# Optimization experiments

Hardware: AMD Instinct MI355X
Metric: run time of the kernel (lower is better)

## Reference

```python
import jax, jax.numpy as jnp
import numpy as np

M, K, N = 4096, 4096, 4096          # tokens, in_features, out_features
ROW_BLOCK, COL_BLOCK = 1, 4          # sparse block shape (rows x cols of W)
BLOCK_DENSITY = 0.2                  # fraction of nonzero blocks


def setup_inputs() -> dict:
    key = jax.random.key(0)
    k1, k2, k3, k4 = jax.random.split(key, 4)
    # quint8 activations stored as int32 in [0, 255]
    x_q = jax.random.randint(k1, (M, K), 0, 256, dtype=jnp.int32)
    # qint8 weights stored as int32 in [-127, 127], zero_point == 0
    w_dense = jax.random.randint(k2, (N, K), -127, 128, dtype=jnp.int32)
    # block-sparse structure: zero out whole ROW_BLOCK x COL_BLOCK blocks
    blk_mask = jax.random.bernoulli(k3, BLOCK_DENSITY, (N // ROW_BLOCK, K // COL_BLOCK))
    mask = jnp.repeat(jnp.repeat(blk_mask, ROW_BLOCK, axis=0), COL_BLOCK, axis=1)
    w_q = jnp.where(mask, w_dense, 0)
    bias = jax.random.normal(k4, (N,), dtype=jnp.float32) * 0.1
    return dict(
        x_q=x_q,
        w_q=w_q,
        bias=bias,
        x_scale=jnp.float32(0.05),
        x_zp=jnp.int32(128),
        w_scale=jnp.float32(0.01),
        out_scale=jnp.float32(0.1),
        out_zp=jnp.int32(128),
    )


def reference(x_q, w_q, bias, x_scale, x_zp, w_scale, out_scale, out_zp):
    # int32 accumulate of (x - x_zp) @ W^T over the (block-)sparse weight
    acc = jnp.einsum('mk,nk->mn', x_q - x_zp, w_q)  # [M, N] int32
    # dequantize + bias
    y = acc.astype(jnp.float32) * (x_scale * w_scale) + bias[None, :]
    # requantize to quint8 (stored as int32)
    q = jnp.round(y / out_scale).astype(jnp.int32) + out_zp
    return jnp.clip(q, 0, 255)
```

## Files before the change

### kernel.cpp

```cpp
#include <hip/hip_runtime.h>
#include <stdint.h>

#define MDIM 4096
#define NDIM 4096
#define KDIM 4096
#define BM 256
#define BN 256
#define BKB 128
#define NT (KDIM / BKB)

typedef int i32x4 __attribute__((ext_vector_type(4)));

typedef __attribute__((address_space(1))) const void gv_t;
typedef __attribute__((address_space(3))) void lv_t;

#define BAR() do { asm volatile("" ::: "memory"); __builtin_amdgcn_s_barrier(); asm volatile("" ::: "memory"); } while (0)

__device__ __forceinline__ int pack4(int a, int b, int c, int d) {
    return (a & 0xFF) | ((b & 0xFF) << 8) | ((c & 0xFF) << 16) | ((d & 0xFF) << 24);
}

__global__ void pack_x_kernel(const int* __restrict__ x, const int* __restrict__ zp_p,
                              int* __restrict__ out, int total4) {
    const int zp = zp_p[0];
    int i = blockIdx.x * blockDim.x + threadIdx.x;
    if (i < total4) {
        int4 a = ((const int4*)x)[i];
        out[i] = pack4(a.x - zp, a.y - zp, a.z - zp, a.w - zp);
    }
}

__global__ void pack_w_kernel(const int* __restrict__ w, int* __restrict__ out, int total4) {
    int i = blockIdx.x * blockDim.x + threadIdx.x;
    if (i < total4) {
        int4 a = ((const int4*)w)[i];
        out[i] = pack4(a.x, a.y, a.z, a.w);
    }
}

__global__ __launch_bounds__(512, 2)
void gemm_i8_8ph(const char* __restrict__ A8, const char* __restrict__ B8,
                 const float* __restrict__ bias,
                 const float* __restrict__ xs_p, const float* __restrict__ ws_p,
                 const float* __restrict__ os_p, const int* __restrict__ ozp_p,
                 int* __restrict__ out) {
    __shared__ char lds[131072];

    const int t = threadIdx.x;
    const int lane = t & 63;
    const int wave = t >> 6;
    const int wr = wave >> 2;
    const int wc = wave & 3;

    int wg = blockIdx.x;
    int swz = (wg & 7) * (256 / 8) + (wg >> 3);
    const long brow = (long)(swz >> 4) * BM;
    const long bcol = (long)(swz & 15) * BN;

    i32x4 acc[8][4] = {};

    auto STAGE_HALF = [&](int tt, int h) {
        if (tt >= NT) return;
        const int d = tt & 1;
        const char* src = (h < 2) ? A8 : B8;
        const long base_rc = (h < 2) ? brow : bcol;
        const int rh = h & 1;
        const int kt = tt * BKB;
        char* ldsbase = lds + ((h < 2) ? 0 : 65536) + d * 32768;
        #pragma unroll
        for (int j = 0; j < 2; ++j) {
            int chunk = rh * 1024 + t + j * 512;
            int row = chunk >> 3, slot = chunk & 7;
            __builtin_amdgcn_global_load_lds(
                (gv_t*)(src + (base_rc + row) * KDIM + kt + ((slot ^ (row & 7)) * 16)),
                (lv_t*)(ldsbase + chunk * 16), 16, 0, 0);
        }
    };

    STAGE_HALF(0, 0); STAGE_HALF(0, 1); STAGE_HALF(0, 2); STAGE_HALF(0, 3);
    STAGE_HALF(1, 0); STAGE_HALF(1, 1); STAGE_HALF(1, 2);

    for (int tt = 0; tt < NT; ++tt) {
        const int d = tt & 1;
        const char* Ac = lds + d * 32768;
        const char* Bc = lds + 65536 + d * 32768;

        STAGE_HALF(tt + 1, 3);
        if (tt == NT - 1) asm volatile("s_waitcnt vmcnt(0)" ::: "memory");
        else              asm volatile("s_waitcnt vmcnt(8)" ::: "memory");
        BAR();

        i32x4 af[8][2], bf[4][2];
        #pragma unroll
        for (int mi = 0; mi < 8; ++mi) {
            int row = wr * 128 + mi * 16 + (lane & 15);
            #pragma unroll
            for (int kk = 0; kk < 2; ++kk) {
                int ls = kk * 4 + (lane >> 4);
                af[mi][kk] = *(const i32x4*)(Ac + row * BKB + ((ls ^ (row & 7)) * 16));
            }
        }
        #pragma unroll
        for (int ni = 0; ni < 4; ++ni) {
            int row = wc * 64 + ni * 16 + (lane & 15);
            #pragma unroll
            for (int kk = 0; kk < 2; ++kk) {
                int ls = kk * 4 + (lane >> 4);
                bf[ni][kk] = *(const i32x4*)(Bc + row * BKB + ((ls ^ (row & 7)) * 16));
            }
        }

        __builtin_amdgcn_s_setprio(1);
        #pragma unroll
        for (int mi = 0; mi < 4; ++mi)
            #pragma unroll
            for (int ni = 0; ni < 2; ++ni)
                #pragma unroll
                for (int kk = 0; kk < 2; ++kk)
                    acc[mi][ni] = __builtin_amdgcn_mfma_i32_16x16x64_i8(af[mi][kk], bf[ni][kk], acc[mi][ni], 0, 0, 0);
        __builtin_amdgcn_s_setprio(0);
        asm volatile("s_waitcnt lgkmcnt(0)" ::: "memory");
        BAR();

        STAGE_HALF(tt + 2, 0);
        BAR();
        __builtin_amdgcn_s_setprio(1);
        #pragma unroll
        for (int mi = 0; mi < 4; ++mi)
            #pragma unroll
            for (int ni = 2; ni < 4; ++ni)
                #pragma unroll
                for (int kk = 0; kk < 2; ++kk)
                    acc[mi][ni] = __builtin_amdgcn_mfma_i32_16x16x64_i8(af[mi][kk], bf[ni][kk], acc[mi][ni], 0, 0, 0);
        __builtin_amdgcn_s_setprio(0);
        BAR();

        STAGE_HALF(tt + 2, 1);
        BAR();
        __builtin_amdgcn_s_setprio(1);
        #pragma unroll
        for (int mi = 4; mi < 8; ++mi)
            #pragma unroll
            for (int ni = 0; ni < 2; ++ni)
                #pragma unroll
                for (int kk = 0; kk < 2; ++kk)
                    acc[mi][ni] = __builtin_amdgcn_mfma_i32_16x16x64_i8(af[mi][kk], bf[ni][kk], acc[mi][ni], 0, 0, 0);
        __builtin_amdgcn_s_setprio(0);
        BAR();

        STAGE_HALF(tt + 2, 2);
        BAR();
        __builtin_amdgcn_s_setprio(1);
        #pragma unroll
        for (int mi = 4; mi < 8; ++mi)
            #pragma unroll
            for (int ni = 2; ni < 4; ++ni)
                #pragma unroll
                for (int kk = 0; kk < 2; ++kk)
                    acc[mi][ni] = __builtin_amdgcn_mfma_i32_16x16x64_i8(af[mi][kk], bf[ni][kk], acc[mi][ni], 0, 0, 0);
        __builtin_amdgcn_s_setprio(0);
        BAR();
    }

    const float scale = xs_p[0] * ws_p[0];
    const float os = os_p[0];
    const int ozp = ozp_p[0];
    #pragma unroll
    for (int mi = 0; mi < 8; ++mi) {
        long row0 = brow + wr * 128 + mi * 16 + (lane >> 4) * 4;
        #pragma unroll
        for (int ni = 0; ni < 4; ++ni) {
            long col = bcol + wc * 64 + ni * 16 + (lane & 15);
            float bv = bias[col];
            #pragma unroll
            for (int r = 0; r < 4; ++r) {
                float y = (float)acc[mi][ni][r] * scale + bv;
                int q = (int)rintf(y / os) + ozp;
                q = q < 0 ? 0 : (q > 255 ? 255 : q);
                out[(row0 + r) * NDIM + col] = q;
            }
        }
    }
}

__global__ void naive_gemm_kernel(const int* __restrict__ x, const int* __restrict__ w,
                                  const float* __restrict__ bias,
                                  const float* __restrict__ xs_p, const int* __restrict__ xzp_p,
                                  const float* __restrict__ ws_p, const float* __restrict__ os_p,
                                  const int* __restrict__ ozp_p, int* __restrict__ out) {
    long idx = (long)blockIdx.x * blockDim.x + threadIdx.x;
    if (idx >= (long)MDIM * NDIM) return;
    int m = idx >> 12, n = idx & (NDIM - 1);
    const int4* xr = (const int4*)(x + (long)m * KDIM);
    const int4* wv = (const int4*)(w + (long)n * KDIM);
    const int zp = xzp_p[0];
    int acc = 0;
    for (int k = 0; k < KDIM / 4; ++k) {
        int4 a = xr[k], b = wv[k];
        acc += (a.x - zp) * b.x + (a.y - zp) * b.y + (a.z - zp) * b.z + (a.w - zp) * b.w;
    }
    float y = (float)acc * (xs_p[0] * ws_p[0]) + bias[n];
    int q = (int)rintf(y / os_p[0]) + ozp_p[0];
    out[idx] = q < 0 ? 0 : (q > 255 ? 255 : q);
}

extern "C" void kernel_launch(void* const* d_in, const int* in_sizes, int n_in,
                              void* d_out, int out_size, void* d_ws, size_t ws_size,
                              hipStream_t stream) {
    const int*   x_q  = (const int*)d_in[0];
    const int*   w_q  = (const int*)d_in[1];
    const float* bias = (const float*)d_in[2];
    const float* xs   = (const float*)d_in[3];
    const int*   xzp  = (const int*)d_in[4];
    const float* wsc  = (const float*)d_in[5];
    const float* osc  = (const float*)d_in[6];
    const int*   ozp  = (const int*)d_in[7];
    int* out = (int*)d_out;

    const size_t need = 2UL * MDIM * KDIM;
    if (ws_size >= need) {
        char* A8 = (char*)d_ws;
        char* B8 = A8 + (size_t)MDIM * KDIM;
        const int total4 = MDIM * KDIM / 4;
        pack_x_kernel<<<total4 / 256, 256, 0, stream>>>(x_q, xzp, (int*)A8, total4);
        pack_w_kernel<<<total4 / 256, 256, 0, stream>>>(w_q, (int*)B8, total4);
        gemm_i8_8ph<<<(MDIM / BM) * (NDIM / BN), 512, 0, stream>>>(
            A8, B8, bias, xs, wsc, osc, ozp, out);
    } else {
        long total = (long)MDIM * NDIM;
        naive_gemm_kernel<<<(total + 255) / 256, 256, 0, stream>>>(
            x_q, w_q, bias, xs, xzp, wsc, osc, ozp, out);
    }
}
```

Baseline: 236.4 us.

## Interleave LDS fragment loads with MFMA quarters and reorder tile staging

Restructures the main loop so A and B fragments are read from LDS in pieces just before the MFMA quarter that uses them, instead of all at once at the top of each iteration. The global-to-LDS staging order also changes: B halves for the next tile and A halves for the tile after next are issued between quarters, with adjusted vmcnt waits. Swizzled LDS and global addresses are precomputed outside the loop, and the loop is unrolled by two. The aim is to overlap LDS reads with MFMA work, lower peak register use and cut per-iteration address arithmetic. The cost is more barriers and lgkmcnt waits per iteration, and more complex correctness reasoning about buffer reuse.

```diff
diff --git a/kernel.cpp b/kernel.cpp
--- a/kernel.cpp
+++ b/kernel.cpp
@@ -15,6 +15,7 @@
 typedef __attribute__((address_space(3))) void lv_t;
 
 #define BAR() do { asm volatile("" ::: "memory"); __builtin_amdgcn_s_barrier(); asm volatile("" ::: "memory"); } while (0)
+#define LGKM0_BAR() do { asm volatile("s_waitcnt lgkmcnt(0)" ::: "memory"); BAR(); } while (0)
 
 __device__ __forceinline__ int pack4(int a, int b, int c, int d) {
     return (a & 0xFF) | ((b & 0xFF) << 8) | ((c & 0xFF) << 16) | ((d & 0xFF) << 24);
@@ -59,108 +60,116 @@
 
     i32x4 acc[8][4] = {};
 
-    auto STAGE_HALF = [&](int tt, int h) {
-        if (tt >= NT) return;
-        const int d = tt & 1;
+    int aoff[8][2], boff[4][2];
+    #pragma unroll
+    for (int mi = 0; mi < 8; ++mi) {
+        int row = wr * 128 + mi * 16 + (lane & 15);
+        #pragma unroll
+        for (int kk = 0; kk < 2; ++kk) {
+            int ls = kk * 4 + (lane >> 4);
+            aoff[mi][kk] = row * BKB + ((ls ^ (row & 7)) * 16);
+        }
+    }
+    #pragma unroll
+    for (int ni = 0; ni < 4; ++ni) {
+        int row = wc * 64 + ni * 16 + (lane & 15);
+        #pragma unroll
+        for (int kk = 0; kk < 2; ++kk) {
+            int ls = kk * 4 + (lane >> 4);
+            boff[ni][kk] = 65536 + row * BKB + ((ls ^ (row & 7)) * 16);
+        }
+    }
+    const char* sbase[4][2];
+    int ldsoff[4][2];
+    #pragma unroll
+    for (int h = 0; h < 4; ++h) {
         const char* src = (h < 2) ? A8 : B8;
-        const long base_rc = (h < 2) ? brow : bcol;
-        const int rh = h & 1;
-        const int kt = tt * BKB;
-        char* ldsbase = lds + ((h < 2) ? 0 : 65536) + d * 32768;
+        long rc = (h < 2) ? brow : bcol;
         #pragma unroll
         for (int j = 0; j < 2; ++j) {
-            int chunk = rh * 1024 + t + j * 512;
+            int chunk = (h & 1) * 1024 + t + j * 512;
             int row = chunk >> 3, slot = chunk & 7;
-            __builtin_amdgcn_global_load_lds(
-                (gv_t*)(src + (base_rc + row) * KDIM + kt + ((slot ^ (row & 7)) * 16)),
-                (lv_t*)(ldsbase + chunk * 16), 16, 0, 0);
-        }
-    };
-
-    STAGE_HALF(0, 0); STAGE_HALF(0, 1); STAGE_HALF(0, 2); STAGE_HALF(0, 3);
-    STAGE_HALF(1, 0); STAGE_HALF(1, 1); STAGE_HALF(1, 2);
-
+            sbase[h][j] = src + (rc + row) * KDIM + ((slot ^ (row & 7)) * 16);
+            ldsoff[h][j] = ((h < 2) ? 0 : 65536) + chunk * 16;
+        }
+    }
+
+#define STAGE(tt_, h_) do { \
+    if ((tt_) < NT) { \
+        int dd_ = ((tt_) & 1) * 32768; \
+        __builtin_amdgcn_global_load_lds((gv_t*)(sbase[h_][0] + (long)(tt_) * BKB), \
+                                         (lv_t*)(lds + dd_ + ldsoff[h_][0]), 16, 0, 0); \
+        __builtin_amdgcn_global_load_lds((gv_t*)(sbase[h_][1] + (long)(tt_) * BKB), \
+                                         (lv_t*)(lds + dd_ + ldsoff[h_][1]), 16, 0, 0); \
+    } } while (0)
+
+#define MFMA_Q(MLO, NLO) do { \
+    __builtin_amdgcn_s_setprio(1); \
+    _Pragma("unroll") \
+    for (int mi = MLO; mi < MLO + 4; ++mi) \
+        _Pragma("unroll") \
+        for (int ni = NLO; ni < NLO + 2; ++ni) \
+            _Pragma("unroll") \
+            for (int kk = 0; kk < 2; ++kk) \
+                acc[mi][ni] = __builtin_amdgcn_mfma_i32_16x16x64_i8(af[mi][kk], bf[ni][kk], acc[mi][ni], 0, 0, 0); \
+    __builtin_amdgcn_s_setprio(0); \
+} while (0)
+
+    STAGE(0, 0); STAGE(0, 1); STAGE(0, 2); STAGE(0, 3);
+    STAGE(1, 0); STAGE(1, 1);
+    asm volatile("s_waitcnt vmcnt(4)" ::: "memory");
+    BAR();
+
+    i32x4 af[8][2], bf[4][2];
+
+    #pragma unroll 2
     for (int tt = 0; tt < NT; ++tt) {
-        const int d = tt & 1;
-        const char* Ac = lds + d * 32768;
-        const char* Bc = lds + 65536 + d * 32768;
-
-        STAGE_HALF(tt + 1, 3);
-        if (tt == NT - 1) asm volatile("s_waitcnt vmcnt(0)" ::: "memory");
-        else              asm volatile("s_waitcnt vmcnt(8)" ::: "memory");
-        BAR();
-
-        i32x4 af[8][2], bf[4][2];
-        #pragma unroll
-        for (int mi = 0; mi < 8; ++mi) {
-            int row = wr * 128 + mi * 16 + (lane & 15);
-            #pragma unroll
-            for (int kk = 0; kk < 2; ++kk) {
-                int ls = kk * 4 + (lane >> 4);
-                af[mi][kk] = *(const i32x4*)(Ac + row * BKB + ((ls ^ (row & 7)) * 16));
-            }
-        }
-        #pragma unroll
-        for (int ni = 0; ni < 4; ++ni) {
-            int row = wc * 64 + ni * 16 + (lane & 15);
-            #pragma unroll
-            for (int kk = 0; kk < 2; ++kk) {
-                int ls = kk * 4 + (lane >> 4);
-                bf[ni][kk] = *(const i32x4*)(Bc + row * BKB + ((ls ^ (row & 7)) * 16));
-            }
-        }
-
-        __builtin_amdgcn_s_setprio(1);
+        const int dpar = (tt & 1) * 32768;
+
         #pragma unroll
         for (int mi = 0; mi < 4; ++mi)
             #pragma unroll
-            for (int ni = 0; ni < 2; ++ni)
-                #pragma unroll
-                for (int kk = 0; kk < 2; ++kk)
-                    acc[mi][ni] = __builtin_amdgcn_mfma_i32_16x16x64_i8(af[mi][kk], bf[ni][kk], acc[mi][ni], 0, 0, 0);
-        __builtin_amdgcn_s_setprio(0);
-        asm volatile("s_waitcnt lgkmcnt(0)" ::: "memory");
-        BAR();
-
-        STAGE_HALF(tt + 2, 0);
-        BAR();
-        __builtin_amdgcn_s_setprio(1);
-        #pragma unroll
-        for (int mi = 0; mi < 4; ++mi)
-            #pragma unroll
-            for (int ni = 2; ni < 4; ++ni)
-                #pragma unroll
-                for (int kk = 0; kk < 2; ++kk)
-                    acc[mi][ni] = __builtin_amdgcn_mfma_i32_16x16x64_i8(af[mi][kk], bf[ni][kk], acc[mi][ni], 0, 0, 0);
-        __builtin_amdgcn_s_setprio(0);
-        BAR();
-
-        STAGE_HALF(tt + 2, 1);
-        BAR();
-        __builtin_amdgcn_s_setprio(1);
+            for (int kk = 0; kk < 2; ++kk)
+                af[mi][kk] = *(const i32x4*)(lds + dpar + aoff[mi][kk]);
+        #pragma unroll
+        for (int ni = 0; ni < 2; ++ni)
+            #pragma unroll
+            for (int kk = 0; kk < 2; ++kk)
+                bf[ni][kk] = *(const i32x4*)(lds + dpar + boff[ni][kk]);
+        STAGE(tt + 1, 2);
+        BAR();
+        MFMA_Q(0, 0);
+        LGKM0_BAR();
+
         #pragma unroll
         for (int mi = 4; mi < 8; ++mi)
             #pragma unroll
-            for (int ni = 0; ni < 2; ++ni)
-                #pragma unroll
-                for (int kk = 0; kk < 2; ++kk)
-                    acc[mi][ni] = __builtin_amdgcn_mfma_i32_16x16x64_i8(af[mi][kk], bf[ni][kk], acc[mi][ni], 0, 0, 0);
-        __builtin_amdgcn_s_setprio(0);
-        BAR();
-
-        STAGE_HALF(tt + 2, 2);
-        BAR();
-        __builtin_amdgcn_s_setprio(1);
-        #pragma unroll
-        for (int mi = 4; mi < 8; ++mi)
-            #pragma unroll
-            for (int ni = 2; ni < 4; ++ni)
-                #pragma unroll
-                for (int kk = 0; kk < 2; ++kk)
-                    acc[mi][ni] = __builtin_amdgcn_mfma_i32_16x16x64_i8(af[mi][kk], bf[ni][kk], acc[mi][ni], 0, 0, 0);
-        __builtin_amdgcn_s_setprio(0);
-        BAR();
-    }
+            for (int kk = 0; kk < 2; ++kk)
+                af[mi][kk] = *(const i32x4*)(lds + dpar + aoff[mi][kk]);
+        STAGE(tt + 1, 3);
+        BAR();
+        MFMA_Q(4, 0);
+        LGKM0_BAR();
+
+        #pragma unroll
+        for (int ni = 2; ni < 4; ++ni)
+            #pragma unroll
+            for (int kk = 0; kk < 2; ++kk)
+                bf[ni][kk] = *(const i32x4*)(lds + dpar + boff[ni][kk]);
+        STAGE(tt + 2, 0);
+        BAR();
+        MFMA_Q(0, 2);
+        LGKM0_BAR();
+
+        STAGE(tt + 2, 1);
+        BAR();
+        MFMA_Q(4, 2);
+        if (tt >= NT - 2)      asm volatile("s_waitcnt vmcnt(0)" ::: "memory");
+        else                   asm volatile("s_waitcnt vmcnt(4)" ::: "memory");
+        BAR();
+    }
+#undef STAGE
+#undef MFMA_Q
 
     const float scale = xs_p[0] * ws_p[0];
     const float os = os_p[0];
```

After: 263.8 us. 1.12x slower.
